# Optimization experiments

Measured on AMD Instinct MI355X. Metric: run time of the kernel, lower is better.

## Reference

```python
import jax, jax.numpy as jnp
import numpy as np

# Crossbar / quantization constants (module defaults: bit_slice=2, bit_stream=1,
# weight_bits=input_bits=acm_bits=16, fracs = 3/4*bits = 12, XBAR_ROW_SIZE=128,
# adc_bit = log2(128) + bit_slice = 9)
XBAR_ROW = 128
WEIGHT_BITS = 16
INPUT_BITS = 16
BIT_SLICE = 2
BIT_STREAM = 1
WFRAC = 12
IFRAC = 12
ACM_BITS = 16
ACM_FRAC = 12
NSLICE = WEIGHT_BITS // BIT_SLICE      # 8 weight bit-slices (MSB-first)
NSTREAM = INPUT_BITS // BIT_STREAM     # 16 input bit streams (LSB-first)
ADC_BIT = int(np.log2(XBAR_ROW)) + BIT_SLICE  # 9


def _fix(v, frac, bits):
    # float -> fixed point integer (2's complement range), int32
    return jnp.clip(jnp.round(v * 2.0 ** frac),
                    -2.0 ** (bits - 1), 2.0 ** (bits - 1) - 1).astype(jnp.int32)


def _mvm_sim(x, weight):
    """Memristor crossbar MVM simulation: bit-sliced weights, bit-streamed inputs,
    per-tile analog sums quantized by an ADC, shift-add accumulation, and
    accumulator-precision output quantization."""
    B, in_f = x.shape
    out_f = weight.shape[0]

    # ---- weights: fixed point 2's complement, sliced into 2-bit slices (MSB slice signed)
    wq = _fix(weight, WFRAC, WEIGHT_BITS)                      # [out, in]
    uw = jnp.where(wq < 0, wq + 2 ** WEIGHT_BITS, wq)          # unsigned 2's complement
    shifts = jnp.array(BIT_SLICE * (NSLICE - 1 - np.arange(NSLICE)))
    sl = (uw[:, :, None] >> shifts) & (2 ** BIT_SLICE - 1)     # [out, in, 8] MSB-first
    msb = sl[:, :, 0]
    sl = sl.at[:, :, 0].set(msb - (2 ** BIT_SLICE) * (msb >> (BIT_SLICE - 1)))  # signed MSB slice

    n_tiles = -(-in_f // XBAR_ROW)
    pad_r = n_tiles * XBAR_ROW - in_f
    W = jnp.pad(sl.transpose(1, 0, 2), ((0, pad_r), (0, 0), (0, 0))).astype(jnp.float32)
    W = W.reshape(n_tiles, XBAR_ROW, out_f, NSLICE)            # [tiles, 128, out, 8]

    # ---- inputs: fixed point 2's complement, streamed one bit at a time (MSB bit negative)
    xq = _fix(x, IFRAC, INPUT_BITS)
    ux = jnp.where(xq < 0, xq + 2 ** INPUT_BITS, xq)
    bits = (ux[:, :, None] >> jnp.arange(NSTREAM)) & 1         # [B, in, 16] LSB-first
    bits = jnp.pad(bits, ((0, 0), (0, pad_r), (0, 0))).astype(jnp.float32)
    bits = bits.reshape(B, n_tiles, XBAR_ROW, NSTREAM).transpose(3, 0, 1, 2)  # [16, B, tiles, 128]

    sw = 2.0 ** np.arange(NSTREAM)
    sw[-1] *= -1.0                                             # 2's complement sign bit
    sw = jnp.asarray(sw, jnp.float32)

    # ADC clipping range per slice (signed range for the signed MSB slice)
    lo = jnp.array([-2.0 ** (ADC_BIT - 1)] + [0.0] * (NSLICE - 1), jnp.float32)
    hi = jnp.array([2.0 ** (ADC_BIT - 1) - 1] + [2.0 ** ADC_BIT - 1] * (NSLICE - 1), jnp.float32)
    slice_w = jnp.asarray(2.0 ** (BIT_SLICE * (NSLICE - 1 - np.arange(NSLICE))), jnp.float32)

    def body(acc, inp):
        b, s = inp                                             # b: [B, tiles, 128]
        partial = jnp.einsum('btr,trok->btok', b, W)           # analog per-tile per-slice sums
        partial = jnp.clip(partial, lo, hi)                    # ADC quantization (clip)
        dig = jnp.einsum('btok,k->bo', partial, slice_w)       # shift-add slices + sum tiles
        return acc + s * dig, None

    acc, _ = jax.lax.scan(body, jnp.zeros((B, out_f), jnp.float32), (bits, sw))

    y = acc * 2.0 ** (-(WFRAC + IFRAC))
    # accumulator precision quantization
    y = jnp.clip(jnp.round(y * 2.0 ** ACM_FRAC),
                 -2.0 ** (ACM_BITS - 1), 2.0 ** (ACM_BITS - 1) - 1) * 2.0 ** (-ACM_FRAC)
    return y


def setup_inputs() -> dict:
    key = jax.random.key(0)
    k1, k2, k3 = jax.random.split(key, 3)
    x = jax.random.normal(k1, (512, 1024), jnp.float32)
    w = jax.random.normal(k2, (1024, 1024), jnp.float32) * 0.05
    b = jax.random.uniform(k3, (1024,), jnp.float32, minval=-0.1, maxval=0.1)
    return {"input": x, "weight": w, "bias": b}


def reference(input, weight, bias):
    return _mvm_sim(input, weight) + bias[None, :]
```

## Files before the change

### kernel.cpp

```cpp
#include <hip/hip_runtime.h>
#include <stdint.h>

typedef int i32x4 __attribute__((ext_vector_type(4)));
typedef float f32x4 __attribute__((ext_vector_type(4)));
typedef unsigned int u32x4 __attribute__((ext_vector_type(4)));

#define B_DIM 512
#define IN_DIM 1024
#define OUT_DIM 1024
#define TM 64
#define TN 32
#define KC 256

__global__ __launch_bounds__(512, 1) void fused_kernel(const float* __restrict__ x,
                                                       const float* __restrict__ w,
                                                       const float* __restrict__ bias,
                                                       float* __restrict__ out) {
    __shared__ signed char sA[2][2 * 64 * 256];
    __shared__ signed char sB[2][2 * 32 * 256];

    int bid = blockIdx.x;
    int nblk = (bid & 7) * 4 + ((bid >> 3) & 3);
    int mblk = bid >> 5;
    int m0 = mblk * TM, n0 = nblk * TN;

    int t = threadIdx.x;
    int lane = t & 63;
    int wv = t >> 6;
    int wm = wv >> 1, wn = wv & 1;

    auto loadc = [&](int c, f32x4 (&v)[3][4]) {
#pragma unroll
        for (int i = 0; i < 2; ++i) {
            int item = i * 512 + t;
            int row = item >> 4, g = item & 15;
            const f32x4* p = (const f32x4*)(x + (size_t)(m0 + row) * IN_DIM + c * KC + g * 16);
#pragma unroll
            for (int j = 0; j < 4; ++j) v[i][j] = p[j];
        }
        {
            int row = t >> 4, g = t & 15;
            const f32x4* p = (const f32x4*)(w + (size_t)(n0 + row) * IN_DIM + c * KC + g * 16);
#pragma unroll
            for (int j = 0; j < 4; ++j) v[2][j] = p[j];
        }
    };

    auto writec = [&](int buf, f32x4 (&v)[3][4]) {
        const float MAGIC = 12583040.0f;
#pragma unroll
        for (int i = 0; i < 3; ++i) {
            const bool isA = i < 2;
            int item = isA ? (i * 512 + t) : t;
            int row = item >> 4, g = item & 15;
            unsigned int hw[4], lw[4];
#pragma unroll
            for (int j = 0; j < 4; ++j) {
                unsigned int tb[4];
#pragma unroll
                for (int e = 0; e < 4; ++e)
                    tb[e] = __builtin_bit_cast(unsigned int,
                                fmaf(v[i][j][e], 4096.0f, MAGIC));
                unsigned p01h = __builtin_amdgcn_perm(tb[1], tb[0], 0x00000501u);
                unsigned p23h = __builtin_amdgcn_perm(tb[3], tb[2], 0x00000501u);
                hw[j] = __builtin_amdgcn_perm(p23h, p01h, 0x05040100u);
                unsigned p01l = __builtin_amdgcn_perm(tb[1], tb[0], 0x00000400u);
                unsigned p23l = __builtin_amdgcn_perm(tb[3], tb[2], 0x00000400u);
                lw[j] = __builtin_amdgcn_perm(p23l, p01l, 0x05040100u) ^ 0x80808080u;
            }
            signed char* base = isA ? &sA[buf][0] : &sB[buf][0];
            int planeStride = isA ? 16384 : 8192;
            int off = row * 256 + ((g ^ (row & 7)) * 16);
            *(u32x4*)(base + off) = *(const u32x4*)hw;
            *(u32x4*)(base + planeStride + off) = *(const u32x4*)lw;
        }
    };

    i32x4 hh = {}, mid = {}, ll = {};
    int arow = wm * 16 + (lane & 15);
    int brow = wn * 16 + (lane & 15);

    auto compute = [&](int buf) {
#pragma unroll
        for (int k4 = 0; k4 < 4; ++k4) {
            int slot = ((k4 * 4 + (lane >> 4)) ^ (lane & 7)) * 16;
            i32x4 a0 = *(const i32x4*)&sA[buf][arow * 256 + slot];
            i32x4 a1 = *(const i32x4*)&sA[buf][16384 + arow * 256 + slot];
            i32x4 b0 = *(const i32x4*)&sB[buf][brow * 256 + slot];
            i32x4 b1 = *(const i32x4*)&sB[buf][8192 + brow * 256 + slot];
            hh  = __builtin_amdgcn_mfma_i32_16x16x64_i8(a0, b0, hh, 0, 0, 0);
            mid = __builtin_amdgcn_mfma_i32_16x16x64_i8(a0, b1, mid, 0, 0, 0);
            mid = __builtin_amdgcn_mfma_i32_16x16x64_i8(a1, b0, mid, 0, 0, 0);
            ll  = __builtin_amdgcn_mfma_i32_16x16x64_i8(a1, b1, ll, 0, 0, 0);
        }
    };

    {
        f32x4 v0[3][4];
        loadc(0, v0);
        writec(0, v0);
    }
    __syncthreads();

#pragma unroll
    for (int c = 0; c < 4; ++c) {
        int buf = c & 1;
        f32x4 vn[3][4];
        if (c < 3) loadc(c + 1, vn);
        compute(buf);
        if (c < 3) writec(buf ^ 1, vn);
        __syncthreads();
    }

    int grow0 = m0 + wm * 16 + ((lane >> 4) << 2);
    int gcol = n0 + wn * 16 + (lane & 15);
    float bv = bias[gcol];
#pragma unroll
    for (int j = 0; j < 4; ++j) {
        int s = hh[j] * 65536 + mid[j] * 256 + ll[j];
        double q = rint((double)s * 0x1p-12);
        q = q < -32768.0 ? -32768.0 : (q > 32767.0 ? 32767.0 : q);
        out[(size_t)(grow0 + j) * OUT_DIM + gcol] = (float)(q * 0x1p-12) + bv;
    }
}

extern "C" void kernel_launch(void* const* d_in, const int* in_sizes, int n_in,
                              void* d_out, int out_size, void* d_ws, size_t ws_size,
                              hipStream_t stream) {
    const float* x = (const float*)d_in[0];
    const float* w = (const float*)d_in[1];
    const float* bias = (const float*)d_in[2];
    float* out = (float*)d_out;

    fused_kernel<<<256, 512, 0, stream>>>(x, w, bias, out);
}
```

Baseline: 14.45 us.

## Halve K chunk and prefetch two chunks ahead with register double-buffering

Shrinks the K chunk from 256 to 128, halving shared-memory usage per buffer, and keeps two chunks of global loads in flight in registers so each load has about two compute phases to arrive. It also raises wave priority around the MFMA section with s_setprio and skips the final barrier. The cost is twice as many barriers and loop iterations, plus more registers held live for the two prefetch buffers.

```diff
diff --git a/kernel.cpp b/kernel.cpp
--- a/kernel.cpp
+++ b/kernel.cpp
@@ -3,6 +3,7 @@
 
 typedef int i32x4 __attribute__((ext_vector_type(4)));
 typedef float f32x4 __attribute__((ext_vector_type(4)));
+typedef unsigned int u32x2 __attribute__((ext_vector_type(2)));
 typedef unsigned int u32x4 __attribute__((ext_vector_type(4)));
 
 #define B_DIM 512
@@ -10,14 +11,16 @@
 #define OUT_DIM 1024
 #define TM 64
 #define TN 32
-#define KC 256
+#define KC 128
+
+struct Chunk { f32x4 a[4]; f32x4 b[2]; };
 
 __global__ __launch_bounds__(512, 1) void fused_kernel(const float* __restrict__ x,
                                                        const float* __restrict__ w,
                                                        const float* __restrict__ bias,
                                                        float* __restrict__ out) {
-    __shared__ signed char sA[2][2 * 64 * 256];
-    __shared__ signed char sB[2][2 * 32 * 256];
+    __shared__ signed char sA[2][16384];
+    __shared__ signed char sB[2][8192];
 
     int bid = blockIdx.x;
     int nblk = (bid & 7) * 4 + ((bid >> 3) & 3);
@@ -29,51 +32,57 @@
     int wv = t >> 6;
     int wm = wv >> 1, wn = wv & 1;
 
-    auto loadc = [&](int c, f32x4 (&v)[3][4]) {
+    int aRow = t >> 3, aG = t & 7;
+    int bRow = t >> 4, bG = t & 15;
+    const float* aSrc = x + (size_t)(m0 + aRow) * IN_DIM + aG * 16;
+    const float* bSrc = w + (size_t)(n0 + bRow) * IN_DIM + bG * 8;
+    int aOff = aRow * 128 + ((aG ^ (aRow & 7)) * 16);
+    int bOff = bRow * 128 + (((bG >> 1) ^ (bRow & 7)) * 16) + (bG & 1) * 8;
+
+    auto loadc = [&](int c, Chunk& v) {
+        const f32x4* pa = (const f32x4*)(aSrc + c * KC);
 #pragma unroll
-        for (int i = 0; i < 2; ++i) {
-            int item = i * 512 + t;
-            int row = item >> 4, g = item & 15;
-            const f32x4* p = (const f32x4*)(x + (size_t)(m0 + row) * IN_DIM + c * KC + g * 16);
+        for (int j = 0; j < 4; ++j) v.a[j] = pa[j];
+        const f32x4* pb = (const f32x4*)(bSrc + c * KC);
 #pragma unroll
-            for (int j = 0; j < 4; ++j) v[i][j] = p[j];
-        }
-        {
-            int row = t >> 4, g = t & 15;
-            const f32x4* p = (const f32x4*)(w + (size_t)(n0 + row) * IN_DIM + c * KC + g * 16);
-#pragma unroll
-            for (int j = 0; j < 4; ++j) v[2][j] = p[j];
-        }
+        for (int j = 0; j < 2; ++j) v.b[j] = pb[j];
     };
 
-    auto writec = [&](int buf, f32x4 (&v)[3][4]) {
-        const float MAGIC = 12583040.0f;
+    const float MAGIC = 12583040.0f;
+    auto writec = [&](int buf, Chunk& v) {
+        unsigned int hwA[4], lwA[4];
 #pragma unroll
-        for (int i = 0; i < 3; ++i) {
-            const bool isA = i < 2;
-            int item = isA ? (i * 512 + t) : t;
-            int row = item >> 4, g = item & 15;
-            unsigned int hw[4], lw[4];
+        for (int j = 0; j < 4; ++j) {
+            unsigned int tb[4];
 #pragma unroll
-            for (int j = 0; j < 4; ++j) {
-                unsigned int tb[4];
+            for (int e = 0; e < 4; ++e)
+                tb[e] = __builtin_bit_cast(unsigned int, fmaf(v.a[j][e], 4096.0f, MAGIC));
+            unsigned p01h = __builtin_amdgcn_perm(tb[1], tb[0], 0x00000501u);
+            unsigned p23h = __builtin_amdgcn_perm(tb[3], tb[2], 0x00000501u);
+            hwA[j] = __builtin_amdgcn_perm(p23h, p01h, 0x05040100u);
+            unsigned p01l = __builtin_amdgcn_perm(tb[1], tb[0], 0x00000400u);
+            unsigned p23l = __builtin_amdgcn_perm(tb[3], tb[2], 0x00000400u);
+            lwA[j] = __builtin_amdgcn_perm(p23l, p01l, 0x05040100u) ^ 0x80808080u;
+        }
+        *(u32x4*)&sA[buf][aOff] = *(const u32x4*)hwA;
+        *(u32x4*)&sA[buf][8192 + aOff] = *(const u32x4*)lwA;
+
+        unsigned int hwB[2], lwB[2];
 #pragma unroll
-                for (int e = 0; e < 4; ++e)
-                    tb[e] = __builtin_bit_cast(unsigned int,
-                                fmaf(v[i][j][e], 4096.0f, MAGIC));
-                unsigned p01h = __builtin_amdgcn_perm(tb[1], tb[0], 0x00000501u);
-                unsigned p23h = __builtin_amdgcn_perm(tb[3], tb[2], 0x00000501u);
-                hw[j] = __builtin_amdgcn_perm(p23h, p01h, 0x05040100u);
-                unsigned p01l = __builtin_amdgcn_perm(tb[1], tb[0], 0x00000400u);
-                unsigned p23l = __builtin_amdgcn_perm(tb[3], tb[2], 0x00000400u);
-                lw[j] = __builtin_amdgcn_perm(p23l, p01l, 0x05040100u) ^ 0x80808080u;
-            }
-            signed char* base = isA ? &sA[buf][0] : &sB[buf][0];
-            int planeStride = isA ? 16384 : 8192;
-            int off = row * 256 + ((g ^ (row & 7)) * 16);
-            *(u32x4*)(base + off) = *(const u32x4*)hw;
-            *(u32x4*)(base + planeStride + off) = *(const u32x4*)lw;
+        for (int j = 0; j < 2; ++j) {
+            unsigned int tb[4];
+#pragma unroll
+            for (int e = 0; e < 4; ++e)
+                tb[e] = __builtin_bit_cast(unsigned int, fmaf(v.b[j][e], 4096.0f, MAGIC));
+            unsigned p01h = __builtin_amdgcn_perm(tb[1], tb[0], 0x00000501u);
+            unsigned p23h = __builtin_amdgcn_perm(tb[3], tb[2], 0x00000501u);
+            hwB[j] = __builtin_amdgcn_perm(p23h, p01h, 0x05040100u);
+            unsigned p01l = __builtin_amdgcn_perm(tb[1], tb[0], 0x00000400u);
+            unsigned p23l = __builtin_amdgcn_perm(tb[3], tb[2], 0x00000400u);
+            lwB[j] = __builtin_amdgcn_perm(p23l, p01l, 0x05040100u) ^ 0x80808080u;
         }
+        *(u32x2*)&sB[buf][bOff] = *(const u32x2*)hwB;
+        *(u32x2*)&sB[buf][4096 + bOff] = *(const u32x2*)lwB;
     };
 
     i32x4 hh = {}, mid = {}, ll = {};
@@ -81,35 +90,36 @@
     int brow = wn * 16 + (lane & 15);
 
     auto compute = [&](int buf) {
+        __builtin_amdgcn_s_setprio(1);
 #pragma unroll
-        for (int k4 = 0; k4 < 4; ++k4) {
+        for (int k4 = 0; k4 < 2; ++k4) {
             int slot = ((k4 * 4 + (lane >> 4)) ^ (lane & 7)) * 16;
-            i32x4 a0 = *(const i32x4*)&sA[buf][arow * 256 + slot];
-            i32x4 a1 = *(const i32x4*)&sA[buf][16384 + arow * 256 + slot];
-            i32x4 b0 = *(const i32x4*)&sB[buf][brow * 256 + slot];
-            i32x4 b1 = *(const i32x4*)&sB[buf][8192 + brow * 256 + slot];
+            i32x4 a0 = *(const i32x4*)&sA[buf][arow * 128 + slot];
+            i32x4 a1 = *(const i32x4*)&sA[buf][8192 + arow * 128 + slot];
+            i32x4 b0 = *(const i32x4*)&sB[buf][brow * 128 + slot];
+            i32x4 b1 = *(const i32x4*)&sB[buf][4096 + brow * 128 + slot];
             hh  = __builtin_amdgcn_mfma_i32_16x16x64_i8(a0, b0, hh, 0, 0, 0);
             mid = __builtin_amdgcn_mfma_i32_16x16x64_i8(a0, b1, mid, 0, 0, 0);
             mid = __builtin_amdgcn_mfma_i32_16x16x64_i8(a1, b0, mid, 0, 0, 0);
             ll  = __builtin_amdgcn_mfma_i32_16x16x64_i8(a1, b1, ll, 0, 0, 0);
         }
+        __builtin_amdgcn_s_setprio(0);
     };
 
-    {
-        f32x4 v0[3][4];
-        loadc(0, v0);
-        writec(0, v0);
-    }
+    Chunk v0, v1;
+    loadc(0, v0);
+    loadc(1, v1);
+    writec(0, v0);
     __syncthreads();
 
 #pragma unroll
-    for (int c = 0; c < 4; ++c) {
-        int buf = c & 1;
-        f32x4 vn[3][4];
-        if (c < 3) loadc(c + 1, vn);
-        compute(buf);
-        if (c < 3) writec(buf ^ 1, vn);
-        __syncthreads();
+    for (int c = 0; c < 8; ++c) {
+        Chunk& vfree = (c & 1) ? v1 : v0;
+        Chunk& vnext = (c & 1) ? v0 : v1;
+        if (c < 6) loadc(c + 2, vfree);
+        compute(c & 1);
+        if (c < 7) writec((c + 1) & 1, vnext);
+        if (c < 7) __syncthreads();
     }
 
     int grow0 = m0 + wm * 16 + ((lane >> 4) << 2);
```

Measured after the change: 11.88 us. 17.8% less time.
